# Kernel tuning notes

Hardware: AMD Instinct MI355X
Metric: run time of the kernel (lower is better)

Reference implementation:

```python
import jax, jax.numpy as jnp
import numpy as np
from jax import lax

B_SZ, SEQ, D_MODEL, D_STATE, DT_RANK = 4, 4096, 256, 16, 16


def setup_inputs() -> dict:
    key = jax.random.key(0)
    ks = jax.random.split(key, 12)
    d, n, r = D_MODEL, D_STATE, DT_RANK
    inp = {}
    inp["hidden_states"] = jax.random.normal(ks[0], (B_SZ, SEQ, d), jnp.float32)
    inp["in_proj_w"] = jax.random.normal(ks[1], (3 * d, d), jnp.float32) * (d ** -0.5)
    inp["x_proj_w"] = jax.random.normal(ks[2], (r + 2 * n, d), jnp.float32) * (d ** -0.5)
    s = r ** -0.5
    inp["dt_proj_w"] = jax.random.uniform(ks[3], (d, r), jnp.float32, -s, s)
    dt = jnp.exp(jax.random.uniform(ks[4], (d,), jnp.float32) * (np.log(0.1) - np.log(1e-3)) + np.log(1e-3))
    inp["dt_proj_b"] = dt + jnp.log(-jnp.expm1(-dt))  # inverse-softplus init
    inp["A_log"] = jnp.log(jnp.broadcast_to(jnp.arange(1, n + 1, dtype=jnp.float32), (d, n)))
    inp["D"] = jnp.ones((d,), jnp.float32)
    inp["out_proj1_w"] = jax.random.normal(ks[5], (d, d), jnp.float32) * (d ** -0.5)
    inp["conv_x_w"] = jax.random.normal(ks[6], (d, 1, 1), jnp.float32)
    inp["conv_x_b"] = jax.random.normal(ks[7], (d,), jnp.float32) * 0.1
    inp["conv_y_w"] = jax.random.normal(ks[8], (d, 1, 3), jnp.float32) * (3 ** -0.5)
    inp["conv_y_b"] = jax.random.normal(ks[9], (d,), jnp.float32) * 0.1
    inp["conv_z_w"] = jax.random.normal(ks[10], (d, 1, 5), jnp.float32) * (5 ** -0.5)
    inp["conv_z_b"] = jax.random.normal(ks[11], (d,), jnp.float32) * 0.1
    return inp


def _silu(x):
    return x * jax.nn.sigmoid(x)


def _dwconv(x, w, b):
    # x: (b, d, l); w: (d, 1, k) depthwise; 'same' padding (odd k)
    k = w.shape[-1]
    pad = (k - 1) // 2
    out = lax.conv_general_dilated(
        x, w, window_strides=(1,), padding=[(pad, pad)],
        dimension_numbers=("NCH", "OIH", "NCH"), feature_group_count=x.shape[1])
    return out + b[None, :, None]


def _selective_scan(u, delta, A, B, C, D, delta_bias):
    # u, delta: (b,d,l); A: (d,n); B,C: (b,n,l); D, delta_bias: (d,)
    delta = jax.nn.softplus(delta + delta_bias[None, :, None])
    dA = jnp.exp(jnp.einsum("bdl,dn->lbdn", delta, A))          # (l,b,d,n)
    dBu = jnp.einsum("bdl,bnl,bdl->lbdn", delta, B, u)           # (l,b,d,n)
    Ct = jnp.transpose(C, (2, 0, 1))                             # (l,b,n)

    def step(h, inp):
        dA_t, dBu_t, C_t = inp
        h = dA_t * h + dBu_t                                     # (b,d,n)
        y = jnp.einsum("bdn,bn->bd", h, C_t)
        return h, y

    h0 = jnp.zeros(u.shape[:2] + (A.shape[1],), u.dtype)
    _, ys = lax.scan(step, h0, (dA, dBu, Ct))                    # ys: (l,b,d)
    y = jnp.transpose(ys, (1, 2, 0))                             # (b,d,l)
    return y + D[None, :, None] * u


def reference(hidden_states, in_proj_w, x_proj_w, dt_proj_w, dt_proj_b, A_log, D,
              out_proj1_w, conv_x_w, conv_x_b, conv_y_w, conv_y_b, conv_z_w, conv_z_b):
    b, l, d = hidden_states.shape
    xyz = jnp.einsum("ble,de->bdl", hidden_states, in_proj_w)    # (b, 3d, l)
    x, y, z = jnp.split(xyz, 3, axis=1)                          # each (b,d,l)
    A = -jnp.exp(A_log.astype(jnp.float32))
    x = _silu(_dwconv(x, conv_x_w, conv_x_b))
    y = _silu(_dwconv(y, conv_y_w, conv_y_b))
    z = _silu(_dwconv(z, conv_z_w, conv_z_b))
    x_dbl = jnp.einsum("bdl,ed->ble", x, x_proj_w)               # (b,l,r+2n)
    dt_r, Bm, Cm = jnp.split(x_dbl, [DT_RANK, DT_RANK + D_STATE], axis=-1)
    # dt_proj applies bias here; selective_scan adds delta_bias again (faithful to source)
    dt = jnp.einsum("blr,dr->bdl", dt_r, dt_proj_w) + dt_proj_b[None, :, None]
    Bm = jnp.transpose(Bm, (0, 2, 1))                            # (b,n,l)
    Cm = jnp.transpose(Cm, (0, 2, 1))
    p = _selective_scan(x, dt, A, Bm, Cm, D.astype(jnp.float32), dt_proj_b.astype(jnp.float32))
    p = jnp.transpose(p, (0, 2, 1))                              # (b,l,d)
    y = jnp.transpose(y, (0, 2, 1))
    z = jnp.transpose(z, (0, 2, 1))
    l1 = jnp.einsum("bld,ed->ble", p * y, out_proj1_w)
    l2 = l1 * z
    l2 = _dwconv(jnp.transpose(l2, (0, 2, 1)), conv_x_w, conv_x_b)
    return jnp.transpose(l2, (0, 2, 1))                          # (b,l,d)
```

## Files before the change

### kernel.cpp

```cpp
#include <hip/hip_runtime.h>
#include <hip/hip_bf16.h>
#include <math.h>

typedef __hip_bfloat16 bf16;
typedef __attribute__((ext_vector_type(8))) short bf16x8;
typedef __attribute__((ext_vector_type(4))) float f32x4;

#define B_SZ 4
#define SEQ  4096
#define DM   256
#define NST  16
#define NCHK 64
#define LC   (SEQ/NCHK)
#define MT   (B_SZ*SEQ)
#define NLIN (B_SZ*16*256)

__device__ __forceinline__ float silu_f(float v){ return v / (1.f + __expf(-v)); }
__device__ __forceinline__ float softplus_f(float v){
  return (v > 15.f) ? v : __logf(1.f + __expf(v));
}
__device__ __forceinline__ short f2bf(float f){
  union { bf16 h; short s; } u; u.h = __float2bfloat16(f); return u.s;
}
__device__ __forceinline__ float bf2f(short s){
  union { unsigned int i; float f; } v;
  v.i = ((unsigned int)(unsigned short)s) << 16; return v.f;
}
__device__ __forceinline__ float4 bf4_to_f4(uint2 q){
  float4 f;
  f.x = bf2f((short)(q.x & 0xffffu)); f.y = bf2f((short)(q.x >> 16));
  f.z = bf2f((short)(q.y & 0xffffu)); f.w = bf2f((short)(q.y >> 16));
  return f;
}
__device__ __forceinline__ short4 f4_to_bf4(float4 f){
  short4 s; s.x = f2bf(f.x); s.y = f2bf(f.y); s.z = f2bf(f.z); s.w = f2bf(f.w);
  return s;
}

__device__ __forceinline__ void async_cp16(const short* g, short* l){
  __builtin_amdgcn_global_load_lds(
      (const __attribute__((address_space(1))) unsigned int*)g,
      (__attribute__((address_space(3))) unsigned int*)l, 16, 0, 0);
}

template<int CTRL>
__device__ __forceinline__ float dpp_add_step(float v){
  int x = __builtin_amdgcn_update_dpp(0, __float_as_int(v), CTRL, 0xf, 0xf, true);
  return v + __int_as_float(x);
}

__global__ __launch_bounds__(256)
void cvt_in_k(const float* __restrict__ w_in, const float* __restrict__ w_o1,
              const float* __restrict__ hs,
              short* __restrict__ w_in_b, short* __restrict__ w_o1_b,
              short* __restrict__ hsb)
{
  int i = blockIdx.x * 256 + threadIdx.x;
  if (i < 49152) {
    float4 q = *(const float4*)&w_in[i * 4];
    *(short4*)&w_in_b[i * 4] = f4_to_bf4(q);
  } else if (i < 65536) {
    int j = i - 49152;
    float4 q = *(const float4*)&w_o1[j * 4];
    *(short4*)&w_o1_b[j * 4] = f4_to_bf4(q);
  } else {
    int j = i - 65536;
    float4 q = *(const float4*)&hs[(size_t)j * 4];
    *(short4*)&hsb[(size_t)j * 4] = f4_to_bf4(q);
  }
}

__global__ __launch_bounds__(256)
void mfma_gemm_conv_k(const short* __restrict__ Av,
                      const short* __restrict__ Bw,
                      const float* __restrict__ wx, const float* __restrict__ bx,
                      const float* __restrict__ wy, const float* __restrict__ by,
                      const float* __restrict__ wz, const float* __restrict__ bz,
                      short* __restrict__ xout, short* __restrict__ yout,
                      short* __restrict__ zout)
{
  constexpr int RM = 80;
  __shared__ __align__(16) char smem_c[26624];
  short* As = (short*)smem_c;
  short* Bs = (short*)(smem_c + 10240);
  const int tid  = threadIdx.x;
  const int wave = tid >> 6, lane = tid & 63;
  const int quad = lane >> 4, l16 = lane & 15;
  const int wn = wave * 32;
  const int m0 = blockIdx.x * 64, n0 = blockIdx.y * 128;

  f32x4 acc[5][2] = {};

  for (int k0 = 0; k0 < 256; k0 += 64) {
    #pragma unroll
    for (int p = 0; p < 3; p++) {
      int id = p * 256 + tid;
      if (id < RM * 8) {
        int row = id >> 3, slot = id & 7;
        int gch = slot ^ (row & 7);
        int gm = m0 - 8 + row;
        gm = gm < 0 ? 0 : (gm > MT - 1 ? MT - 1 : gm);
        async_cp16(Av + (size_t)gm * 256 + k0 + gch * 8,
                   &As[row * 64 + slot * 8]);
      }
    }
    #pragma unroll
    for (int p = 0; p < 4; p++) {
      int id = p * 256 + tid;
      int row = id >> 3, slot = id & 7;
      int gch = slot ^ (row & 7);
      async_cp16(Bw + (size_t)(n0 + row) * 256 + k0 + gch * 8,
                 &Bs[row * 64 + slot * 8]);
    }
    __syncthreads();
    #pragma unroll
    for (int ks = 0; ks < 2; ks++) {
      bf16x8 fa[5], fb[2];
      int sa = (ks * 4 + quad) ^ (l16 & 7);
      #pragma unroll
      for (int i = 0; i < 5; i++)
        fa[i] = *(const bf16x8*)&As[(i * 16 + l16) * 64 + sa * 8];
      #pragma unroll
      for (int j = 0; j < 2; j++)
        fb[j] = *(const bf16x8*)&Bs[(wn + j * 16 + l16) * 64 + sa * 8];
      #pragma unroll
      for (int i = 0; i < 5; i++)
        #pragma unroll
        for (int j = 0; j < 2; j++)
          acc[i][j] = __builtin_amdgcn_mfma_f32_16x16x32_bf16(fa[i], fb[j], acc[i][j], 0, 0, 0);
    }
    __syncthreads();
  }

  short* Ts = (short*)smem_c;
  #pragma unroll
  for (int i = 0; i < 5; i++) {
    #pragma unroll
    for (int j = 0; j < 2; j++) {
      int col = wn + j * 16 + l16;
      int row = i * 16 + quad * 4;
      short4 v;
      v.x = f2bf(acc[i][j][0]); v.y = f2bf(acc[i][j][1]);
      v.z = f2bf(acc[i][j][2]); v.w = f2bf(acc[i][j][3]);
      *(short4*)&Ts[col * 84 + row] = v;
    }
  }
  __syncthreads();

  const int cp = tid & 63, rg = tid >> 6;
  const int lc0 = cp * 2;
  const int lr0 = rg * 16;
  const int lbase = (m0 & (SEQ - 1)) + lr0;
  float ta[24], tb[24];
  {
    const short* q0 = &Ts[lc0 * 84 + lr0 + 4];
    #pragma unroll
    for (int q = 0; q < 6; q++) {
      short4 a = *(const short4*)&q0[q * 4];
      short4 b = *(const short4*)&q0[84 + q * 4];
      ta[q*4+0] = bf2f(a.x); ta[q*4+1] = bf2f(a.y);
      ta[q*4+2] = bf2f(a.z); ta[q*4+3] = bf2f(a.w);
      tb[q*4+0] = bf2f(b.x); tb[q*4+1] = bf2f(b.y);
      tb[q*4+2] = bf2f(b.z); tb[q*4+3] = bf2f(b.w);
    }
  }
  const int type = n0 >> 8;
  const int gq = n0 + lc0 - type * 256;
  if (type == 0) {
    float w0 = wx[gq], w1 = wx[gq + 1];
    float b0 = bx[gq], b1 = bx[gq + 1];
    #pragma unroll
    for (int t = 0; t < 16; t++) {
      short2 o;
      o.x = f2bf(silu_f(fmaf(ta[t + 4], w0, b0)));
      o.y = f2bf(silu_f(fmaf(tb[t + 4], w1, b1)));
      *(short2*)&xout[(size_t)(m0 + lr0 + t) * 256 + gq] = o;
    }
  } else if (type == 1) {
    float w0[3], w1[3];
    #pragma unroll
    for (int j = 0; j < 3; j++) { w0[j] = wy[gq*3 + j]; w1[j] = wy[(gq+1)*3 + j]; }
    float b0 = by[gq], b1 = by[gq + 1];
    #pragma unroll
    for (int t = 0; t < 16; t++) {
      float a0 = b0, a1 = b1;
      #pragma unroll
      for (int j = 0; j < 3; j++) {
        int l = lbase + t + j - 1;
        bool ok = ((unsigned)l < SEQ);
        a0 = fmaf(ok ? ta[t + 3 + j] : 0.f, w0[j], a0);
        a1 = fmaf(ok ? tb[t + 3 + j] : 0.f, w1[j], a1);
      }
      short2 o; o.x = f2bf(silu_f(a0)); o.y = f2bf(silu_f(a1));
      *(short2*)&yout[(size_t)(m0 + lr0 + t) * 256 + gq] = o;
    }
  } else {
    float w0[5], w1[5];
    #pragma unroll
    for (int j = 0; j < 5; j++) { w0[j] = wz[gq*5 + j]; w1[j] = wz[(gq+1)*5 + j]; }
    float b0 = bz[gq], b1 = bz[gq + 1];
    #pragma unroll
    for (int t = 0; t < 16; t++) {
      float a0 = b0, a1 = b1;
      #pragma unroll
      for (int j = 0; j < 5; j++) {
        int l = lbase + t + j - 2;
        bool ok = ((unsigned)l < SEQ);
        a0 = fmaf(ok ? ta[t + 2 + j] : 0.f, w0[j], a0);
        a1 = fmaf(ok ? tb[t + 2 + j] : 0.f, w1[j], a1);
      }
      short2 o; o.x = f2bf(silu_f(a0)); o.y = f2bf(silu_f(a1));
      *(short2*)&zout[(size_t)(m0 + lr0 + t) * 256 + gq] = o;
    }
  }
}

template<int EPI, bool OBF, int BM>
__global__ __launch_bounds__(256)
void mfma_gemm_k(const short* __restrict__ Av, const short* __restrict__ Bw,
                 void* __restrict__ Outv, int N, int K,
                 const float* __restrict__ bias, const short* __restrict__ zc,
                 const float* __restrict__ cwx)
{
  constexpr int BN = 128, BK = 64;
  constexpr int JF = (BM == 64) ? 2 : 4;
  __shared__ short As[BM * BK];
  __shared__ short Bs[BN * BK];
  const int tid  = threadIdx.x;
  const int wave = tid >> 6, lane = tid & 63;
  const int quad = lane >> 4, l16 = lane & 15;
  const int wm = (BM == 64) ? 0 : (wave & 1) * 64;
  const int wn = (BM == 64) ? wave * 32 : (wave >> 1) * 64;
  const int m0 = blockIdx.x * BM, n0 = blockIdx.y * BN;

  f32x4 acc[4][JF] = {};

  for (int k0 = 0; k0 < K; k0 += BK) {
    #pragma unroll
    for (int p = 0; p < BM * 8 / 256; p++) {
      int id = p * 256 + tid;
      int row = id >> 3, slot = id & 7;
      int gch = slot ^ (row & 7);
      async_cp16(Av + (size_t)(m0 + row) * K + k0 + gch * 8,
                 &As[row * 64 + slot * 8]);
    }
    #pragma unroll
    for (int p = 0; p < 4; p++) {
      int id = p * 256 + tid;
      int row = id >> 3, slot = id & 7;
      int gch = slot ^ (row & 7);
      async_cp16(Bw + (size_t)(n0 + row) * K + k0 + gch * 8,
                 &Bs[row * 64 + slot * 8]);
    }
    __syncthreads();
    #pragma unroll
    for (int ks = 0; ks < 2; ks++) {
      bf16x8 fa[4], fb[JF];
      int sa = (ks * 4 + quad) ^ (l16 & 7);
      #pragma unroll
      for (int i = 0; i < 4; i++)
        fa[i] = *(const bf16x8*)&As[(wm + i * 16 + l16) * 64 + sa * 8];
      #pragma unroll
      for (int j = 0; j < JF; j++)
        fb[j] = *(const bf16x8*)&Bs[(wn + j * 16 + l16) * 64 + sa * 8];
      #pragma unroll
      for (int i = 0; i < 4; i++)
        #pragma unroll
        for (int j = 0; j < JF; j++)
          acc[i][j] = __builtin_amdgcn_mfma_f32_16x16x32_bf16(fa[i], fb[j], acc[i][j], 0, 0, 0);
    }
    __syncthreads();
  }

  #pragma unroll
  for (int i = 0; i < 4; i++) {
    #pragma unroll
    for (int j = 0; j < JF; j++) {
      int n = n0 + wn + j * 16 + l16;
      #pragma unroll
      for (int r = 0; r < 4; r++) {
        int m = m0 + wm + i * 16 + quad * 4 + r;
        float v = acc[i][j][r];
        if constexpr (EPI == 2)
          v = v * bf2f(zc[(size_t)m * N + n]) * cwx[n] + bias[n];
        if constexpr (OBF) ((short*)Outv)[(size_t)m * N + n] = f2bf(v);
        else               ((float*)Outv)[(size_t)m * N + n] = v;
      }
    }
  }
}

__global__ __launch_bounds__(256)
void gemm34_k(const short* __restrict__ xcb,
              const float* __restrict__ Bw,
              const float* __restrict__ wdt,
              const float* __restrict__ bdt,
              float* __restrict__ xdbl,
              float* __restrict__ dtv)
{
  constexpr int TM = 32, TK = 16, NN = 48;
  __shared__ __align__(16) float As[TK][TM + 4];
  __shared__ __align__(16) float Bs[TK][64 + 4];
  __shared__ __align__(16) float dt_s[TM][20];
  __shared__ __align__(16) float wdt_s[256][20];
  const int tid = threadIdx.x;
  const int tn = tid & 15, tm = tid >> 4;
  const int m0 = blockIdx.x * TM;
  float acc[2][4] = {};
  const int mlA = tid >> 3, kdA = (tid & 7) * 2;
  const int mlB = tid >> 2, kqB = (tid & 3) * 4;

  {
    float4 q0 = *(const float4*)&wdt[tid * 16 + 0];
    float4 q1 = *(const float4*)&wdt[tid * 16 + 4];
    float4 q2 = *(const float4*)&wdt[tid * 16 + 8];
    float4 q3 = *(const float4*)&wdt[tid * 16 + 12];
    *(float4*)&wdt_s[tid][0]  = q0;
    *(float4*)&wdt_s[tid][4]  = q1;
    *(float4*)&wdt_s[tid][8]  = q2;
    *(float4*)&wdt_s[tid][12] = q3;
  }

  for (int k0 = 0; k0 < 256; k0 += TK) {
    {
      size_t off = (size_t)(m0 + mlA) * 256 + k0 + kdA;
      unsigned int v = *(const unsigned int*)(xcb + off);
      As[kdA + 0][mlA] = bf2f((short)(v & 0xffffu));
      As[kdA + 1][mlA] = bf2f((short)(v >> 16));
    }
    {
      float v0 = 0.f, v1 = 0.f, v2 = 0.f, v3 = 0.f;
      if (mlB < NN) {
        float4 q = *(const float4*)(Bw + (size_t)mlB * 256 + k0 + kqB);
        v0 = q.x; v1 = q.y; v2 = q.z; v3 = q.w;
      }
      Bs[kqB+0][mlB] = v0; Bs[kqB+1][mlB] = v1; Bs[kqB+2][mlB] = v2; Bs[kqB+3][mlB] = v3;
    }
    __syncthreads();
    #pragma unroll
    for (int k = 0; k < TK; k++) {
      float2 av = *(const float2*)&As[k][tm << 1];
      float4 bv = *(const float4*)&Bs[k][tn << 2];
      float a[2] = {av.x, av.y};
      float b[4] = {bv.x, bv.y, bv.z, bv.w};
      #pragma unroll
      for (int i = 0; i < 2; i++)
        #pragma unroll
        for (int j = 0; j < 4; j++)
          acc[i][j] = fmaf(a[i], b[j], acc[i][j]);
    }
    __syncthreads();
  }

  #pragma unroll
  for (int i = 0; i < 2; i++) {
    int m = m0 + (tm << 1) + i;
    #pragma unroll
    for (int j = 0; j < 4; j++) {
      int n = (tn << 2) + j;
      float v = acc[i][j];
      if (n < NN) xdbl[(size_t)m * NN + n] = v;
      if (tn < 4) dt_s[(tm << 1) + i][n] = v;
    }
  }
  __syncthreads();

  const int c0 = tid & 63, rg = tid >> 6;
  float w[4][16];
  float bb[4];
  #pragma unroll
  for (int cc = 0; cc < 4; cc++) {
    int col = cc * 64 + c0;
    #pragma unroll
    for (int q = 0; q < 4; q++) {
      float4 t = *(const float4*)&wdt_s[col][q * 4];
      w[cc][q*4+0] = t.x; w[cc][q*4+1] = t.y; w[cc][q*4+2] = t.z; w[cc][q*4+3] = t.w;
    }
    bb[cc] = 2.f * bdt[col];
  }
  #pragma unroll
  for (int rr = 0; rr < 8; rr++) {
    int row = rg * 8 + rr;
    float dr[16];
    #pragma unroll
    for (int q = 0; q < 4; q++) {
      float4 t = *(const float4*)&dt_s[row][q * 4];
      dr[q*4+0] = t.x; dr[q*4+1] = t.y; dr[q*4+2] = t.z; dr[q*4+3] = t.w;
    }
    #pragma unroll
    for (int cc = 0; cc < 4; cc++) {
      float s = bb[cc];
      #pragma unroll
      for (int k = 0; k < 16; k++) s = fmaf(dr[k], w[cc][k], s);
      dtv[(size_t)(m0 + row) * 256 + cc * 64 + c0] = softplus_f(s);
    }
  }
}

template<bool PASSC>
__global__ __launch_bounds__(256)
void scan_k(const short* __restrict__ xcb,
            const float* __restrict__ dtv,
            const float* __restrict__ xdbl,
            const float* __restrict__ A_log,
            const float* __restrict__ Dp,
            const float* __restrict__ Hstart,
            float* __restrict__ Pbuf, float* __restrict__ hfbuf,
            const short* __restrict__ ycb,
            short* __restrict__ poutb)
{
  __shared__ __align__(16) float2 du2_s[16 * 66];
  __shared__ __align__(16) float2 BC_s [PASSC ? 16 * 66 : 2];
  __shared__ __align__(16) float  Bc_s [PASSC ? 4 : 16 * 68];
  __shared__ __align__(16) float  y_s  [PASSC ? 16 * 68 : 4];
  const int tid = threadIdx.x;
  const int n = tid & 15, dl = tid >> 4;
  const int ch = blockIdx.x;
  const int d0 = blockIdx.y * 16;
  const int b  = blockIdx.z;
  const int d  = d0 + dl;
  const int t0 = ch * LC;
  const size_t brow = (size_t)b * SEQ;
  const size_t cidx = (size_t)ch * NLIN + ((size_t)b * 16 + blockIdx.y) * 256 + tid;

  float u_r[4];
  #pragma unroll
  for (int i = 0; i < 4; i++) {
    int t = (tid >> 4) + i * 16;
    int dd = tid & 15;
    size_t row = brow + t0 + t;
    float uval = bf2f(xcb[row * 256 + d0 + dd]);
    float dval = dtv[row * 256 + d0 + dd];
    du2_s[dd * 66 + t] = make_float2(dval, dval * uval);
    if constexpr (PASSC) {
      BC_s[dd * 66 + t] = make_float2(xdbl[row * 48 + 16 + dd],
                                      xdbl[row * 48 + 32 + dd]);
      u_r[i] = uval;
    } else {
      Bc_s[dd * 68 + t] = xdbl[row * 48 + 16 + dd];
    }
  }
  __syncthreads();

  const float A_dn = -__expf(A_log[d * NST + n]);

  float h = PASSC ? Hstart[cidx] : 0.f;
  float P = 1.f;
  for (int t4 = 0; t4 < LC; t4 += 4) {
    float4 a = *(const float4*)&du2_s[dl * 66 + t4];
    float4 c = *(const float4*)&du2_s[dl * 66 + t4 + 2];
    float dA[4], du[4];
    dA[0] = __expf(a.x * A_dn); du[0] = a.y;
    dA[1] = __expf(a.z * A_dn); du[1] = a.w;
    dA[2] = __expf(c.x * A_dn); du[2] = c.y;
    dA[3] = __expf(c.z * A_dn); du[3] = c.w;
    if constexpr (!PASSC) {
      float4 f = *(const float4*)&Bc_s[n * 68 + t4];
      float Bv[4] = {f.x, f.y, f.z, f.w};
      #pragma unroll
      for (int j = 0; j < 4; j++) {
        h = fmaf(dA[j], h, du[j] * Bv[j]);
        P *= dA[j];
      }
    } else {
      float4 e = *(const float4*)&BC_s[n * 66 + t4];
      float4 g = *(const float4*)&BC_s[n * 66 + t4 + 2];
      float Bv[4] = {e.x, e.z, g.x, g.z};
      float Cv[4] = {e.y, e.w, g.y, g.w};
      float yv[4];
      #pragma unroll
      for (int j = 0; j < 4; j++) {
        h = fmaf(dA[j], h, du[j] * Bv[j]);
        yv[j] = h * Cv[j];
      }
      #pragma unroll
      for (int j = 0; j < 4; j++) yv[j] = dpp_add_step<0x118>(yv[j]);
      #pragma unroll
      for (int j = 0; j < 4; j++) yv[j] = dpp_add_step<0x114>(yv[j]);
      #pragma unroll
      for (int j = 0; j < 4; j++) yv[j] = dpp_add_step<0x112>(yv[j]);
      #pragma unroll
      for (int j = 0; j < 4; j++) yv[j] = dpp_add_step<0x111>(yv[j]);
      if (n == 15)
        *(float4*)&y_s[dl * 68 + t4] = make_float4(yv[0], yv[1], yv[2], yv[3]);
    }
  }

  if constexpr (!PASSC) {
    Pbuf[cidx] = P;
    hfbuf[cidx] = h;
  } else {
    __syncthreads();
    const float Dval = Dp[d0 + n];
    #pragma unroll
    for (int i = 0; i < 4; i++) {
      int t = (tid >> 4) + i * 16;
      size_t row = brow + t0 + t;
      float p = fmaf(Dval, u_r[i], y_s[n * 68 + t]);
      float yg = bf2f(ycb[row * 256 + d0 + n]);
      poutb[row * 256 + d0 + n] = f2bf(p * yg);
    }
  }
}

__global__ __launch_bounds__(256)
void scan_mid_k(const float* __restrict__ Pbuf, const float* __restrict__ hfbuf,
                float* __restrict__ Hstart)
{
  int lin = blockIdx.x * 256 + threadIdx.x;
  float H = 0.f;
  for (int c = 0; c < NCHK; c++) {
    size_t idx = (size_t)c * NLIN + lin;
    Hstart[idx] = H;
    H = Pbuf[idx] * H + hfbuf[idx];
  }
}

extern "C" void kernel_launch(void* const* d_in, const int* in_sizes, int n_in,
                              void* d_out, int out_size, void* d_ws, size_t ws_size,
                              hipStream_t stream)
{
  const float* hs    = (const float*)d_in[0];
  const float* w_in  = (const float*)d_in[1];
  const float* w_xp  = (const float*)d_in[2];
  const float* w_dt  = (const float*)d_in[3];
  const float* b_dt  = (const float*)d_in[4];
  const float* A_log = (const float*)d_in[5];
  const float* Dp    = (const float*)d_in[6];
  const float* w_o1  = (const float*)d_in[7];
  const float* cwx   = (const float*)d_in[8];
  const float* cbx   = (const float*)d_in[9];
  const float* cwy   = (const float*)d_in[10];
  const float* cby   = (const float*)d_in[11];
  const float* cwz   = (const float*)d_in[12];
  const float* cbz   = (const float*)d_in[13];

  char* wsb = (char*)d_ws;
  short* xcb  = (short*)wsb;
  short* ycb  = xcb + (size_t)MT * 256;
  short* zcb  = ycb + (size_t)MT * 256;
  short* pbufb= zcb + (size_t)MT * 256;
  short* w_in_b = pbufb + (size_t)MT * 256;
  short* w_o1_b = w_in_b + 768 * 256;
  short* hsb  = w_o1_b + 256 * 256;
  float* xdbl = (float*)(hsb + (size_t)MT * 256 + 128);
  float* dtv  = xdbl + (size_t)MT * 48;
  float* Pb   = dtv  + (size_t)MT * 256;
  float* hf   = Pb   + (size_t)NCHK * NLIN;
  float* Hs   = hf   + (size_t)NCHK * NLIN;

  dim3 blk(256);

  cvt_in_k<<<dim3(4352), blk, 0, stream>>>(w_in, w_o1, hs, w_in_b, w_o1_b, hsb);

  mfma_gemm_conv_k<<<dim3(MT / 64, 768 / 128), blk, 0, stream>>>(
      hsb, w_in_b, cwx, cbx, cwy, cby, cwz, cbz, xcb, ycb, zcb);

  gemm34_k<<<dim3(MT / 32), blk, 0, stream>>>(
      xcb, w_xp, w_dt, b_dt, xdbl, dtv);

  scan_k<false><<<dim3(NCHK, DM / 16, B_SZ), blk, 0, stream>>>(
      xcb, dtv, xdbl, A_log, Dp, nullptr, Pb, hf, nullptr, nullptr);
  scan_mid_k<<<dim3(NLIN / 256), blk, 0, stream>>>(Pb, hf, Hs);
  scan_k<true><<<dim3(NCHK, DM / 16, B_SZ), blk, 0, stream>>>(
      xcb, dtv, xdbl, A_log, Dp, Hs, nullptr, nullptr, ycb, pbufb);

  mfma_gemm_k<2, false, 64><<<dim3(MT / 64, 256 / 128), blk, 0, stream>>>(
      pbufb, w_o1_b, d_out, 256, 256, cbx, zcb, cwx);
}
```

Before: 188.8 us.

## Fuse dt projection into scan kernels and derive chunk decay from summed dt

Removes the dt_proj GEMM and softplus from the xdbl kernel and recomputes them inside both scan passes from the 16-wide dt rank slice, eliminating the fp32 (MT x 256) dtv buffer write and its two reads. The first scan pass now stores the per-channel sum of dt instead of the per-state product of decays, and the mid kernel rebuilds the chunk decay as exp2(A*sum), shrinking that buffer by a factor of 16. exp is also switched to a native exp2 with a prescaled A. The trade-off is the dt projection being computed twice, plus a small numerical difference from reconstructing the decay product.

```diff
diff --git a/kernel.cpp b/kernel.cpp
--- a/kernel.cpp
+++ b/kernel.cpp
@@ -14,6 +14,8 @@
 #define LC   (SEQ/NCHK)
 #define MT   (B_SZ*SEQ)
 #define NLIN (B_SZ*16*256)
+
+#define LOG2E 1.4426950408889634f
 
 __device__ __forceinline__ float silu_f(float v){ return v / (1.f + __expf(-v)); }
 __device__ __forceinline__ float softplus_f(float v){
@@ -291,35 +293,19 @@
 }
 
 __global__ __launch_bounds__(256)
-void gemm34_k(const short* __restrict__ xcb,
-              const float* __restrict__ Bw,
-              const float* __restrict__ wdt,
-              const float* __restrict__ bdt,
-              float* __restrict__ xdbl,
-              float* __restrict__ dtv)
+void gemm3_k(const short* __restrict__ xcb,
+             const float* __restrict__ Bw,
+             float* __restrict__ xdbl)
 {
   constexpr int TM = 32, TK = 16, NN = 48;
   __shared__ __align__(16) float As[TK][TM + 4];
   __shared__ __align__(16) float Bs[TK][64 + 4];
-  __shared__ __align__(16) float dt_s[TM][20];
-  __shared__ __align__(16) float wdt_s[256][20];
   const int tid = threadIdx.x;
   const int tn = tid & 15, tm = tid >> 4;
   const int m0 = blockIdx.x * TM;
   float acc[2][4] = {};
   const int mlA = tid >> 3, kdA = (tid & 7) * 2;
   const int mlB = tid >> 2, kqB = (tid & 3) * 4;
-
-  {
-    float4 q0 = *(const float4*)&wdt[tid * 16 + 0];
-    float4 q1 = *(const float4*)&wdt[tid * 16 + 4];
-    float4 q2 = *(const float4*)&wdt[tid * 16 + 8];
-    float4 q3 = *(const float4*)&wdt[tid * 16 + 12];
-    *(float4*)&wdt_s[tid][0]  = q0;
-    *(float4*)&wdt_s[tid][4]  = q1;
-    *(float4*)&wdt_s[tid][8]  = q2;
-    *(float4*)&wdt_s[tid][12] = q3;
-  }
 
   for (int k0 = 0; k0 < 256; k0 += TK) {
     {
@@ -358,41 +344,7 @@
     #pragma unroll
     for (int j = 0; j < 4; j++) {
       int n = (tn << 2) + j;
-      float v = acc[i][j];
-      if (n < NN) xdbl[(size_t)m * NN + n] = v;
-      if (tn < 4) dt_s[(tm << 1) + i][n] = v;
-    }
-  }
-  __syncthreads();
-
-  const int c0 = tid & 63, rg = tid >> 6;
-  float w[4][16];
-  float bb[4];
-  #pragma unroll
-  for (int cc = 0; cc < 4; cc++) {
-    int col = cc * 64 + c0;
-    #pragma unroll
-    for (int q = 0; q < 4; q++) {
-      float4 t = *(const float4*)&wdt_s[col][q * 4];
-      w[cc][q*4+0] = t.x; w[cc][q*4+1] = t.y; w[cc][q*4+2] = t.z; w[cc][q*4+3] = t.w;
-    }
-    bb[cc] = 2.f * bdt[col];
-  }
-  #pragma unroll
-  for (int rr = 0; rr < 8; rr++) {
-    int row = rg * 8 + rr;
-    float dr[16];
-    #pragma unroll
-    for (int q = 0; q < 4; q++) {
-      float4 t = *(const float4*)&dt_s[row][q * 4];
-      dr[q*4+0] = t.x; dr[q*4+1] = t.y; dr[q*4+2] = t.z; dr[q*4+3] = t.w;
-    }
-    #pragma unroll
-    for (int cc = 0; cc < 4; cc++) {
-      float s = bb[cc];
-      #pragma unroll
-      for (int k = 0; k < 16; k++) s = fmaf(dr[k], w[cc][k], s);
-      dtv[(size_t)(m0 + row) * 256 + cc * 64 + c0] = softplus_f(s);
+      if (n < NN) xdbl[(size_t)m * NN + n] = acc[i][j];
     }
   }
 }
@@ -400,12 +352,13 @@
 template<bool PASSC>
 __global__ __launch_bounds__(256)
 void scan_k(const short* __restrict__ xcb,
-            const float* __restrict__ dtv,
             const float* __restrict__ xdbl,
+            const float* __restrict__ wdtp,
+            const float* __restrict__ bdtp,
             const float* __restrict__ A_log,
             const float* __restrict__ Dp,
             const float* __restrict__ Hstart,
-            float* __restrict__ Pbuf, float* __restrict__ hfbuf,
+            float* __restrict__ Sdt, float* __restrict__ hfbuf,
             const short* __restrict__ ycb,
             short* __restrict__ poutb)
 {
@@ -413,6 +366,7 @@
   __shared__ __align__(16) float2 BC_s [PASSC ? 16 * 66 : 2];
   __shared__ __align__(16) float  Bc_s [PASSC ? 4 : 16 * 68];
   __shared__ __align__(16) float  y_s  [PASSC ? 16 * 68 : 4];
+  __shared__ __align__(16) float  dtR_s[64 * 20];
   const int tid = threadIdx.x;
   const int n = tid & 15, dl = tid >> 4;
   const int ch = blockIdx.x;
@@ -423,45 +377,76 @@
   const size_t brow = (size_t)b * SEQ;
   const size_t cidx = (size_t)ch * NLIN + ((size_t)b * 16 + blockIdx.y) * 256 + tid;
 
+  float wr[16];
+  {
+    const float* wp = wdtp + (size_t)(d0 + n) * 16;
+    float4 q0 = *(const float4*)&wp[0];
+    float4 q1 = *(const float4*)&wp[4];
+    float4 q2 = *(const float4*)&wp[8];
+    float4 q3 = *(const float4*)&wp[12];
+    wr[0]=q0.x; wr[1]=q0.y; wr[2]=q0.z; wr[3]=q0.w;
+    wr[4]=q1.x; wr[5]=q1.y; wr[6]=q1.z; wr[7]=q1.w;
+    wr[8]=q2.x; wr[9]=q2.y; wr[10]=q2.z; wr[11]=q2.w;
+    wr[12]=q3.x; wr[13]=q3.y; wr[14]=q3.z; wr[15]=q3.w;
+  }
+  const float b2 = 2.f * bdtp[d0 + n];
+
   float u_r[4];
   #pragma unroll
   for (int i = 0; i < 4; i++) {
-    int t = (tid >> 4) + i * 16;
-    int dd = tid & 15;
+    int t = dl + i * 16;
     size_t row = brow + t0 + t;
-    float uval = bf2f(xcb[row * 256 + d0 + dd]);
-    float dval = dtv[row * 256 + d0 + dd];
-    du2_s[dd * 66 + t] = make_float2(dval, dval * uval);
+    u_r[i] = bf2f(xcb[row * 256 + d0 + n]);
+    dtR_s[t * 20 + n] = xdbl[row * 48 + n];
     if constexpr (PASSC) {
-      BC_s[dd * 66 + t] = make_float2(xdbl[row * 48 + 16 + dd],
-                                      xdbl[row * 48 + 32 + dd]);
-      u_r[i] = uval;
+      BC_s[n * 66 + t] = make_float2(xdbl[row * 48 + 16 + n],
+                                     xdbl[row * 48 + 32 + n]);
     } else {
-      Bc_s[dd * 68 + t] = xdbl[row * 48 + 16 + dd];
+      Bc_s[n * 68 + t] = xdbl[row * 48 + 16 + n];
     }
   }
   __syncthreads();
 
-  const float A_dn = -__expf(A_log[d * NST + n]);
+  #pragma unroll
+  for (int i = 0; i < 4; i++) {
+    int t = dl + i * 16;
+    float4 r0 = *(const float4*)&dtR_s[t * 20 + 0];
+    float4 r1 = *(const float4*)&dtR_s[t * 20 + 4];
+    float4 r2 = *(const float4*)&dtR_s[t * 20 + 8];
+    float4 r3 = *(const float4*)&dtR_s[t * 20 + 12];
+    float s = b2;
+    s = fmaf(r0.x, wr[0], s);  s = fmaf(r0.y, wr[1], s);
+    s = fmaf(r0.z, wr[2], s);  s = fmaf(r0.w, wr[3], s);
+    s = fmaf(r1.x, wr[4], s);  s = fmaf(r1.y, wr[5], s);
+    s = fmaf(r1.z, wr[6], s);  s = fmaf(r1.w, wr[7], s);
+    s = fmaf(r2.x, wr[8], s);  s = fmaf(r2.y, wr[9], s);
+    s = fmaf(r2.z, wr[10], s); s = fmaf(r2.w, wr[11], s);
+    s = fmaf(r3.x, wr[12], s); s = fmaf(r3.y, wr[13], s);
+    s = fmaf(r3.z, wr[14], s); s = fmaf(r3.w, wr[15], s);
+    float sp = softplus_f(s);
+    du2_s[n * 66 + t] = make_float2(sp, sp * u_r[i]);
+  }
+  __syncthreads();
+
+  const float A2 = -__expf(A_log[d * NST + n]) * LOG2E;
 
   float h = PASSC ? Hstart[cidx] : 0.f;
-  float P = 1.f;
+  float sdt = 0.f;
   for (int t4 = 0; t4 < LC; t4 += 4) {
     float4 a = *(const float4*)&du2_s[dl * 66 + t4];
     float4 c = *(const float4*)&du2_s[dl * 66 + t4 + 2];
     float dA[4], du[4];
-    dA[0] = __expf(a.x * A_dn); du[0] = a.y;
-    dA[1] = __expf(a.z * A_dn); du[1] = a.w;
-    dA[2] = __expf(c.x * A_dn); du[2] = c.y;
-    dA[3] = __expf(c.z * A_dn); du[3] = c.w;
+    dA[0] = __builtin_amdgcn_exp2f(a.x * A2); du[0] = a.y;
+    dA[1] = __builtin_amdgcn_exp2f(a.z * A2); du[1] = a.w;
+    dA[2] = __builtin_amdgcn_exp2f(c.x * A2); du[2] = c.y;
+    dA[3] = __builtin_amdgcn_exp2f(c.z * A2); du[3] = c.w;
     if constexpr (!PASSC) {
+      sdt += (a.x + a.z) + (c.x + c.z);
       float4 f = *(const float4*)&Bc_s[n * 68 + t4];
       float Bv[4] = {f.x, f.y, f.z, f.w};
       #pragma unroll
-      for (int j = 0; j < 4; j++) {
+      for (int j = 0; j < 4; j++)
         h = fmaf(dA[j], h, du[j] * Bv[j]);
-        P *= dA[j];
-      }
     } else {
       float4 e = *(const float4*)&BC_s[n * 66 + t4];
       float4 g = *(const float4*)&BC_s[n * 66 + t4 + 2];
@@ -487,14 +472,15 @@
   }
 
   if constexpr (!PASSC) {
-    Pbuf[cidx] = P;
     hfbuf[cidx] = h;
+    if (n == 0)
+      Sdt[((size_t)ch * B_SZ + b) * 256 + d] = sdt;
   } else {
     __syncthreads();
     const float Dval = Dp[d0 + n];
     #pragma unroll
     for (int i = 0; i < 4; i++) {
-      int t = (tid >> 4) + i * 16;
+      int t = dl + i * 16;
       size_t row = brow + t0 + t;
       float p = fmaf(Dval, u_r[i], y_s[n * 68 + t]);
       float yg = bf2f(ycb[row * 256 + d0 + n]);
@@ -503,16 +489,21 @@
   }
 }
 
-__global__ __launch_bounds__(256)
-void scan_mid_k(const float* __restrict__ Pbuf, const float* __restrict__ hfbuf,
-                float* __restrict__ Hstart)
-{
-  int lin = blockIdx.x * 256 + threadIdx.x;
+__global__ __launch_bounds__(64)
+void scan_mid_k(const float* __restrict__ Sdt, const float* __restrict__ hfbuf,
+                const float* __restrict__ A_log, float* __restrict__ Hstart)
+{
+  int lin = blockIdx.x * 64 + threadIdx.x;
+  int b = lin >> 12;
+  int d = (lin >> 4) & 255;
+  int n = lin & 15;
+  const float A2 = -__expf(A_log[d * NST + n]) * LOG2E;
   float H = 0.f;
   for (int c = 0; c < NCHK; c++) {
     size_t idx = (size_t)c * NLIN + lin;
     Hstart[idx] = H;
-    H = Pbuf[idx] * H + hfbuf[idx];
+    float P = __builtin_amdgcn_exp2f(A2 * Sdt[((size_t)c * B_SZ + b) * 256 + d]);
+    H = P * H + hfbuf[idx];
   }
 }
 
@@ -544,9 +535,8 @@
   short* w_o1_b = w_in_b + 768 * 256;
   short* hsb  = w_o1_b + 256 * 256;
   float* xdbl = (float*)(hsb + (size_t)MT * 256 + 128);
-  float* dtv  = xdbl + (size_t)MT * 48;
-  float* Pb   = dtv  + (size_t)MT * 256;
-  float* hf   = Pb   + (size_t)NCHK * NLIN;
+  float* Sdtb = xdbl + (size_t)MT * 48;
+  float* hf   = Sdtb + (size_t)NCHK * B_SZ * 256;
   float* Hs   = hf   + (size_t)NCHK * NLIN;
 
   dim3 blk(256);
@@ -556,14 +546,13 @@
   mfma_gemm_conv_k<<<dim3(MT / 64, 768 / 128), blk, 0, stream>>>(
       hsb, w_in_b, cwx, cbx, cwy, cby, cwz, cbz, xcb, ycb, zcb);
 
-  gemm34_k<<<dim3(MT / 32), blk, 0, stream>>>(
-      xcb, w_xp, w_dt, b_dt, xdbl, dtv);
+  gemm3_k<<<dim3(MT / 32), blk, 0, stream>>>(xcb, w_xp, xdbl);
 
   scan_k<false><<<dim3(NCHK, DM / 16, B_SZ), blk, 0, stream>>>(
-      xcb, dtv, xdbl, A_log, Dp, nullptr, Pb, hf, nullptr, nullptr);
-  scan_mid_k<<<dim3(NLIN / 256), blk, 0, stream>>>(Pb, hf, Hs);
+      xcb, xdbl, w_dt, b_dt, A_log, Dp, nullptr, Sdtb, hf, nullptr, nullptr);
+  scan_mid_k<<<dim3(NLIN / 64), dim3(64), 0, stream>>>(Sdtb, hf, A_log, Hs);
   scan_k<true><<<dim3(NCHK, DM / 16, B_SZ), blk, 0, stream>>>(
-      xcb, dtv, xdbl, A_log, Dp, Hs, nullptr, nullptr, ycb, pbufb);
+      xcb, xdbl, w_dt, b_dt, A_log, Dp, Hs, nullptr, nullptr, ycb, pbufb);
 
   mfma_gemm_k<2, false, 64><<<dim3(MT / 64, 256 / 128), blk, 0, stream>>>(
       pbufb, w_o1_b, d_out, 256, 256, cbx, zcb, cwx);
```

Measured after the change: 199.2 us. 5.5% more time.

## Replace per-chunk decay product with summed dt and use exp2 in scan

Applied to the files above, without the earlier changes.

The chunk-local scan no longer multiplies dA factors into a per-state product P. It accumulates the sum of dt per channel and writes one value per (chunk,b,d) instead of per state, and the mid pass rebuilds P as exp2(A*log2e*sum_dt). Exponentials switch to the hardware exp2 builtin with A prescaled by log2e. The mid kernel also moves to 64-thread blocks to spread its sequential 64-chunk loop over more blocks. This cuts multiplies and global writes and reads of the P buffer, at a small cost in numerical rounding differences.

```diff
diff --git a/kernel.cpp b/kernel.cpp
--- a/kernel.cpp
+++ b/kernel.cpp
@@ -14,6 +14,8 @@
 #define LC   (SEQ/NCHK)
 #define MT   (B_SZ*SEQ)
 #define NLIN (B_SZ*16*256)
+
+#define LOG2E 1.4426950408889634f
 
 __device__ __forceinline__ float silu_f(float v){ return v / (1.f + __expf(-v)); }
 __device__ __forceinline__ float softplus_f(float v){
@@ -405,7 +407,7 @@
             const float* __restrict__ A_log,
             const float* __restrict__ Dp,
             const float* __restrict__ Hstart,
-            float* __restrict__ Pbuf, float* __restrict__ hfbuf,
+            float* __restrict__ Sdt, float* __restrict__ hfbuf,
             const short* __restrict__ ycb,
             short* __restrict__ poutb)
 {
@@ -442,26 +444,25 @@
   }
   __syncthreads();
 
-  const float A_dn = -__expf(A_log[d * NST + n]);
+  const float A2 = -__expf(A_log[d * NST + n]) * LOG2E;
 
   float h = PASSC ? Hstart[cidx] : 0.f;
-  float P = 1.f;
+  float sdt = 0.f;
   for (int t4 = 0; t4 < LC; t4 += 4) {
     float4 a = *(const float4*)&du2_s[dl * 66 + t4];
     float4 c = *(const float4*)&du2_s[dl * 66 + t4 + 2];
     float dA[4], du[4];
-    dA[0] = __expf(a.x * A_dn); du[0] = a.y;
-    dA[1] = __expf(a.z * A_dn); du[1] = a.w;
-    dA[2] = __expf(c.x * A_dn); du[2] = c.y;
-    dA[3] = __expf(c.z * A_dn); du[3] = c.w;
+    dA[0] = __builtin_amdgcn_exp2f(a.x * A2); du[0] = a.y;
+    dA[1] = __builtin_amdgcn_exp2f(a.z * A2); du[1] = a.w;
+    dA[2] = __builtin_amdgcn_exp2f(c.x * A2); du[2] = c.y;
+    dA[3] = __builtin_amdgcn_exp2f(c.z * A2); du[3] = c.w;
     if constexpr (!PASSC) {
+      sdt += (a.x + a.z) + (c.x + c.z);
       float4 f = *(const float4*)&Bc_s[n * 68 + t4];
       float Bv[4] = {f.x, f.y, f.z, f.w};
       #pragma unroll
-      for (int j = 0; j < 4; j++) {
+      for (int j = 0; j < 4; j++)
         h = fmaf(dA[j], h, du[j] * Bv[j]);
-        P *= dA[j];
-      }
     } else {
       float4 e = *(const float4*)&BC_s[n * 66 + t4];
       float4 g = *(const float4*)&BC_s[n * 66 + t4 + 2];
@@ -487,8 +488,9 @@
   }
 
   if constexpr (!PASSC) {
-    Pbuf[cidx] = P;
     hfbuf[cidx] = h;
+    if (n == 0)
+      Sdt[((size_t)ch * B_SZ + b) * 256 + d] = sdt;
   } else {
     __syncthreads();
     const float Dval = Dp[d0 + n];
@@ -503,16 +505,21 @@
   }
 }
 
-__global__ __launch_bounds__(256)
-void scan_mid_k(const float* __restrict__ Pbuf, const float* __restrict__ hfbuf,
-                float* __restrict__ Hstart)
-{
-  int lin = blockIdx.x * 256 + threadIdx.x;
+__global__ __launch_bounds__(64)
+void scan_mid_k(const float* __restrict__ Sdt, const float* __restrict__ hfbuf,
+                const float* __restrict__ A_log, float* __restrict__ Hstart)
+{
+  int lin = blockIdx.x * 64 + threadIdx.x;
+  int b = lin >> 12;
+  int d = (lin >> 4) & 255;
+  int n = lin & 15;
+  const float A2 = -__expf(A_log[d * NST + n]) * LOG2E;
   float H = 0.f;
   for (int c = 0; c < NCHK; c++) {
     size_t idx = (size_t)c * NLIN + lin;
     Hstart[idx] = H;
-    H = Pbuf[idx] * H + hfbuf[idx];
+    float P = __builtin_amdgcn_exp2f(A2 * Sdt[((size_t)c * B_SZ + b) * 256 + d]);
+    H = P * H + hfbuf[idx];
   }
 }
 
@@ -545,8 +552,8 @@
   short* hsb  = w_o1_b + 256 * 256;
   float* xdbl = (float*)(hsb + (size_t)MT * 256 + 128);
   float* dtv  = xdbl + (size_t)MT * 48;
-  float* Pb   = dtv  + (size_t)MT * 256;
-  float* hf   = Pb   + (size_t)NCHK * NLIN;
+  float* Sdtb = dtv  + (size_t)MT * 256;
+  float* hf   = Sdtb + (size_t)NCHK * B_SZ * 256;
   float* Hs   = hf   + (size_t)NCHK * NLIN;
 
   dim3 blk(256);
@@ -560,8 +567,8 @@
       xcb, w_xp, w_dt, b_dt, xdbl, dtv);
 
   scan_k<false><<<dim3(NCHK, DM / 16, B_SZ), blk, 0, stream>>>(
-      xcb, dtv, xdbl, A_log, Dp, nullptr, Pb, hf, nullptr, nullptr);
-  scan_mid_k<<<dim3(NLIN / 256), blk, 0, stream>>>(Pb, hf, Hs);
+      xcb, dtv, xdbl, A_log, Dp, nullptr, Sdtb, hf, nullptr, nullptr);
+  scan_mid_k<<<dim3(NLIN / 64), dim3(64), 0, stream>>>(Sdtb, hf, A_log, Hs);
   scan_k<true><<<dim3(NCHK, DM / 16, B_SZ), blk, 0, stream>>>(
       xcb, dtv, xdbl, A_log, Dp, Hs, nullptr, nullptr, ycb, pbufb);
 
```

New measurement: 195.4 us. +3.5%, slower.
